# Kernel tuning notes

Measured on AMD Instinct MI355X. Metric: run time of the kernel, lower is better.

## Reference

```python
import jax, jax.numpy as jnp
import numpy as np

B, CIN, CGD, CE, G, H, W = 4, 256, 256, 64, 4, 80, 80
N = H * W
EPS = 1e-8


def _build_trees(guide_embed):
    # guide_embed: np [B, CE, N]. Minimum spanning tree on the 4-connected pixel
    # grid with edge cost exp(||e_u - e_v||^2) (exp is monotone -> same MST as
    # squared distance), then BFS order rooted at node 0.
    idx = np.arange(N).reshape(H, W)
    eu = np.concatenate([idx[:, :-1].ravel(), idx[:-1, :].ravel()])
    ev = np.concatenate([idx[:, 1:].ravel(), idx[1:, :].ravel()])
    orders, parents = [], []
    for b in range(B):
        fm = guide_embed[b]
        dist = ((fm[:, eu] - fm[:, ev]) ** 2).sum(0)
        root = np.arange(N)

        def find(x):
            while root[x] != x:
                root[x] = root[root[x]]
                x = root[x]
            return x

        adj = [[] for _ in range(N)]
        cnt = 0
        for e in np.argsort(dist, kind='stable'):
            a, b2 = find(eu[e]), find(ev[e])
            if a != b2:
                root[a] = b2
                adj[eu[e]].append(ev[e])
                adj[ev[e]].append(eu[e])
                cnt += 1
                if cnt == N - 1:
                    break
        order = np.zeros(N, np.int32)   # order[k] = node id at BFS position k
        ppos = np.zeros(N, np.int32)    # ppos[k]  = BFS position of parent of order[k]
        pos = np.zeros(N, np.int32)
        seen = np.zeros(N, bool)
        seen[0] = True
        head, tail = 0, 1
        while head < tail:
            x = order[head]
            for y in adj[x]:
                if not seen[y]:
                    seen[y] = True
                    order[tail] = y
                    pos[y] = tail
                    ppos[tail] = pos[x]
                    tail += 1
            head += 1
        orders.append(order)
        parents.append(ppos)
    return np.stack(orders), np.stack(parents)


def setup_inputs():
    key = jax.random.key(0)
    ks = jax.random.split(key, 7)
    feature = jax.random.normal(ks[0], (B, CIN, H, W), jnp.float32)
    guide = jax.random.normal(ks[1], (B, CGD, H, W), jnp.float32)
    # 1x1 convs == channel matmuls; std=0.01 per module init (conf/beta/gamma
    # are randomized instead of zero so the test is non-trivial)
    W_embed = 0.01 * jax.random.normal(ks[2], (CE, CIN), jnp.float32)
    W_conf = 0.05 * jax.random.normal(ks[3], (G, CIN), jnp.float32)
    W_guide = 0.01 * jax.random.normal(ks[4], (CE, CGD), jnp.float32)
    beta = 0.1 * jax.random.normal(ks[5], (G,), jnp.float32)
    gamma = 0.5 * jax.random.normal(ks[6], (1,), jnp.float32)
    # tree is built under no_grad in the original -> precompute (eval path: MST)
    ge = np.einsum('oc,bcn->bon', np.asarray(W_guide), np.asarray(guide).reshape(B, CGD, N))
    order, parent = _build_trees(ge)
    return {"feature": feature, "guide": guide, "W_embed": W_embed,
            "W_conf": W_conf, "W_guide": W_guide, "beta": beta, "gamma": gamma,
            "order": jnp.asarray(order), "parent": jnp.asarray(parent)}


def _group_edge_dist(x, order, parent):
    # x: [B, CE, N]; per-group squared L2 between each BFS node and its parent
    src = jnp.take_along_axis(x, order[:, None, :], axis=2)
    tgt = jnp.take_along_axis(src, parent[:, None, :], axis=2)
    d = (src - tgt) ** 2
    return d.reshape(B, G, CE // G, N).sum(axis=2)  # [B, G, N]


def _tree_filter(fs, w, parent):
    # fs: [N, G, C] node features in BFS order; w: [N, G] weight of edge to parent
    n = fs.shape[0]

    def up(agg, k):  # leaves -> root: subtree aggregation
        return agg.at[parent[k]].add(w[k][:, None] * agg[k]), None

    agg, _ = jax.lax.scan(up, fs, jnp.arange(n - 1, 0, -1))

    def down(out, k):  # root -> leaves: full-tree aggregation
        wk = w[k][:, None]
        return out.at[k].set(agg[k] + wk * (out[parent[k]] - wk * agg[k])), None

    out, _ = jax.lax.scan(down, agg, jnp.arange(1, n))
    return out


def reference(feature, guide, W_embed, W_conf, W_guide, beta, gamma, order, parent):
    f = feature.reshape(B, CIN, N)
    g = guide.reshape(B, CGD, N)  # adaptive_avg_pool2d to same HxW == identity
    embed = jnp.einsum('oc,bcn->bon', W_embed, f)
    guide_embed = jnp.einsum('oc,bcn->bon', W_guide, g)
    conf = jax.nn.sigmoid(jnp.einsum('gc,bcn->bgn', W_conf, f))  # [B, G, N]

    d_e = _group_edge_dist(embed, order, parent)
    d_g = _group_edge_dist(guide_embed, order, parent)
    # edge weight = exp(-d_embed) * exp(-d_guide) * exp(-beta^2) (self/att term)
    w = jnp.exp(-(d_e + d_g + (beta ** 2)[None, :, None]))  # [B, G, N] by BFS pos

    fg = f.reshape(B, G, CIN // G, N) * conf[:, :, None, :]  # conf-reweighted feat
    x = jnp.concatenate([fg, conf[:, :, None, :]], axis=2)   # filter feat & norm together
    xs = jnp.take_along_axis(x, order[:, None, None, :], axis=3)
    xs = xs.transpose(0, 3, 1, 2)                            # [B, N, G, Cpg+1]
    out = jax.vmap(_tree_filter)(xs, w.transpose(0, 2, 1), parent)
    inv = jnp.argsort(order, axis=1)                         # node -> BFS position
    out = jnp.take_along_axis(out, inv[:, :, None, None], axis=1)
    out = out.transpose(0, 2, 3, 1)                          # [B, G, Cpg+1, N]
    filt, norm = out[:, :, :-1, :], out[:, :, -1:, :]
    res = (filt / (EPS + norm)).reshape(B, CIN, N)
    return (gamma[0] * res + f).reshape(B, CIN, H, W)
```

## Files before the change

kernel.cpp:

```cpp
#include <hip/hip_runtime.h>
#include <math.h>

#define NB    4
#define CINC  256
#define NG    4
#define NPIX  6400
#define NROWS 132
#define CHG   65
#define TEPS  1e-8f
#define TP    128
#define KC    32
#define GT    256
#define SCH   5
#define SPITCH 6413
#define SWT   320
#define PT    640
#define LSC   512

typedef unsigned short u16;
typedef unsigned int   u32;

__global__ __launch_bounds__(PT) void prep_kernel(
    const int* __restrict__ order, const int* __restrict__ parent,
    u16* __restrict__ par16, int* __restrict__ ls,
    int* __restrict__ nl, int* __restrict__ inv)
{
  const int b = blockIdx.x;
  const int tid = threadIdx.x;
  const int* par = parent + b*NPIX;
  const int* ord = order + b*NPIX;
  __shared__ int lvl[NPIX];
  __shared__ int anc[NPIX];
  __shared__ int smax;

  #pragma unroll
  for (int it = 0; it < NPIX/PT; ++it) {
    int k = tid + it*PT;
    int p = par[k];
    lvl[k] = (k == 0) ? 0 : 1;
    anc[k] = p;
    inv[b*NPIX + ord[k]] = k;
    par16[b*NPIX + k] = (u16)p;
  }
  __syncthreads();

  for (int r = 0; r < 13; ++r) {
    int nlv[NPIX/PT], nan_[NPIX/PT];
    #pragma unroll
    for (int it = 0; it < NPIX/PT; ++it) {
      int k = tid + it*PT;
      int a = anc[k];
      nlv[it]  = lvl[k] + lvl[a];
      nan_[it] = anc[a];
    }
    __syncthreads();
    #pragma unroll
    for (int it = 0; it < NPIX/PT; ++it) {
      int k = tid + it*PT;
      lvl[k] = nlv[it];
      anc[k] = nan_[it];
    }
    __syncthreads();
  }

  if (tid == 0) smax = 0;
  __syncthreads();
  int m = 0;
  #pragma unroll
  for (int it = 0; it < NPIX/PT; ++it) m = max(m, lvl[tid + it*PT]);
  atomicMax(&smax, m);
  __syncthreads();
  if (tid == 0) {
    nl[b] = smax + 1;
    ls[b*(NPIX+2) + smax + 1] = NPIX;
  }
  #pragma unroll
  for (int it = 0; it < NPIX/PT; ++it) {
    int k = tid + it*PT;
    if (k == 0 || lvl[k] != lvl[k-1]) ls[b*(NPIX+2) + lvl[k]] = k;
  }
}

__global__ __launch_bounds__(GT) void gemm_kernel(
    const float* __restrict__ f, const float* __restrict__ g,
    const float* __restrict__ We, const float* __restrict__ Wc,
    const float* __restrict__ Wg, float* __restrict__ emb)
{
  const int b  = blockIdx.y;
  const int t0 = blockIdx.x * TP;
  const int tid = threadIdx.x;
  const int i = tid >> 4;
  const int j = tid & 15;

  __shared__ float fT[KC][TP];
  __shared__ float gT[KC][TP];
  __shared__ float wTt[KC][136];

  float acc[8][8];
  #pragma unroll
  for (int r = 0; r < 8; ++r)
    #pragma unroll
    for (int p = 0; p < 8; ++p) acc[r][p] = 0.f;
  float accc[8];
  #pragma unroll
  for (int p = 0; p < 8; ++p) accc[p] = 0.f;

  const float* fb = f + (size_t)b*CINC*NPIX;
  const float* gb = g + (size_t)b*CINC*NPIX;
  const float (*xT)[TP] = (i < 8) ? fT : gT;

  for (int kc = 0; kc < CINC; kc += KC) {
    {
      int kk = tid >> 3;
      int p  = (tid & 7) * 16;
      const float4* srcf = reinterpret_cast<const float4*>(fb + (size_t)(kc+kk)*NPIX + t0 + p);
      const float4* srcg = reinterpret_cast<const float4*>(gb + (size_t)(kc+kk)*NPIX + t0 + p);
      float4* df = reinterpret_cast<float4*>(&fT[kk][p]);
      float4* dg = reinterpret_cast<float4*>(&gT[kk][p]);
      #pragma unroll
      for (int q = 0; q < 4; ++q) { df[q] = srcf[q]; dg[q] = srcg[q]; }
    }
    for (int s = tid; s < 528; s += GT) {
      int r = s >> 2, kb0 = (s & 3) * 8;
      const float* wsrc;
      if (r < 64)       wsrc = We + r*CINC + kc + kb0;
      else if (r < 128) wsrc = Wg + (r-64)*CINC + kc + kb0;
      else              wsrc = Wc + (r-128)*CINC + kc + kb0;
      const float4* wv = reinterpret_cast<const float4*>(wsrc);
      float4 v0 = wv[0], v1 = wv[1];
      wTt[kb0+0][r]=v0.x; wTt[kb0+1][r]=v0.y; wTt[kb0+2][r]=v0.z; wTt[kb0+3][r]=v0.w;
      wTt[kb0+4][r]=v1.x; wTt[kb0+5][r]=v1.y; wTt[kb0+6][r]=v1.z; wTt[kb0+7][r]=v1.w;
    }
    __syncthreads();

    for (int kk = 0; kk < KC; ++kk) {
      float4 x0 = *reinterpret_cast<const float4*>(&xT[kk][4*j]);
      float4 x1 = *reinterpret_cast<const float4*>(&xT[kk][64 + 4*j]);
      float4 w0 = *reinterpret_cast<const float4*>(&wTt[kk][8*i]);
      float4 w1 = *reinterpret_cast<const float4*>(&wTt[kk][8*i + 4]);
#define FMA8(r, wv) \
      acc[r][0] += (wv)*x0.x; acc[r][1] += (wv)*x0.y; acc[r][2] += (wv)*x0.z; acc[r][3] += (wv)*x0.w; \
      acc[r][4] += (wv)*x1.x; acc[r][5] += (wv)*x1.y; acc[r][6] += (wv)*x1.z; acc[r][7] += (wv)*x1.w;
      FMA8(0, w0.x) FMA8(1, w0.y) FMA8(2, w0.z) FMA8(3, w0.w)
      FMA8(4, w1.x) FMA8(5, w1.y) FMA8(6, w1.z) FMA8(7, w1.w)
#undef FMA8
      if (i < 4) {
        float wcf = wTt[kk][128 + i];
        accc[0] += wcf*x0.x; accc[1] += wcf*x0.y; accc[2] += wcf*x0.z; accc[3] += wcf*x0.w;
        accc[4] += wcf*x1.x; accc[5] += wcf*x1.y; accc[6] += wcf*x1.z; accc[7] += wcf*x1.w;
      }
    }
    __syncthreads();
  }

  float* eb = emb + (size_t)b*NPIX*NROWS;
  #pragma unroll
  for (int p = 0; p < 8; ++p) {
    int n = t0 + ((p >> 2) * 64) + 4*j + (p & 3);
    float4 v0 = make_float4(acc[0][p], acc[1][p], acc[2][p], acc[3][p]);
    float4 v1 = make_float4(acc[4][p], acc[5][p], acc[6][p], acc[7][p]);
    float* base = eb + (size_t)n*NROWS + 8*i;
    *reinterpret_cast<float4*>(base)     = v0;
    *reinterpret_cast<float4*>(base + 4) = v1;
    if (i < 4) eb[(size_t)n*NROWS + 128 + i] = 1.f / (1.f + expf(-accc[p]));
  }
}

__global__ __launch_bounds__(256) void wdist_kernel(
    const float* __restrict__ emb, const int* __restrict__ order,
    const int* __restrict__ parent, const float* __restrict__ beta,
    u16* __restrict__ wq)
{
  int idx = blockIdx.x*256 + threadIdx.x;
  int b = idx / NPIX;
  int k = idx - b*NPIX;
  int n  = order[idx];
  int kp = parent[idx];
  int np = order[b*NPIX + kp];
  const float4* e0 = reinterpret_cast<const float4*>(emb + ((size_t)b*NPIX + n )*NROWS);
  const float4* e1 = reinterpret_cast<const float4*>(emb + ((size_t)b*NPIX + np)*NROWS);
  float d[NG] = {0.f, 0.f, 0.f, 0.f};
  #pragma unroll
  for (int q = 0; q < 32; ++q) {
    float4 a = e0[q], c = e1[q];
    int gg = (q & 15) >> 2;
    float t0 = a.x-c.x, t1 = a.y-c.y, t2 = a.z-c.z, t3 = a.w-c.w;
    d[gg] += t0*t0 + t1*t1 + t2*t2 + t3*t3;
  }
  #pragma unroll
  for (int gg = 0; gg < NG; ++gg) {
    float bg = beta[gg];
    float w = expf(-(d[gg] + bg*bg));
    wq[((size_t)(b*NG+gg))*NPIX + k] = (u16)(w*65535.f + 0.5f);
  }
}

__global__ __launch_bounds__(256) void gatherX_kernel(
    const float* __restrict__ f, const float* __restrict__ emb,
    const int* __restrict__ order, float* __restrict__ aggT)
{
  const int bid = blockIdx.x;
  const int pair = bid & 15, tile = bid >> 4;
  const int b = pair >> 2, g = pair & 3;
  const int k0 = tile * 128;
  const int tid = threadIdx.x;

  __shared__ int   s_ord[128];
  __shared__ float s_cf[128];
  if (tid < 128) {
    int n = order[b*NPIX + k0 + tid];
    s_ord[tid] = n;
    s_cf[tid]  = emb[((size_t)b*NPIX + n)*NROWS + 128 + g];
  }
  __syncthreads();

  const float* fb = f + (size_t)b*CINC*NPIX + (size_t)g*64*NPIX;
  float* dst = aggT + (size_t)(b*NG+g)*CHG*NPIX + k0;
  const int c0 = tid >> 7;
  const int j  = tid & 127;
  const int n  = s_ord[j];
  const float cf = s_cf[j];
  #pragma unroll 4
  for (int cc = c0; cc < 64; cc += 2) {
    dst[(size_t)cc*NPIX + j] = fb[(size_t)cc*NPIX + n] * cf;
  }
  if (tid < 128) dst[(size_t)64*NPIX + j] = cf;
}

__global__ __launch_bounds__(SWT, 1) void sweep_kernel(
    float* __restrict__ aggT, const u16* __restrict__ wq,
    const u16* __restrict__ par16, const int* __restrict__ ls,
    const int* __restrict__ nl)
{
  extern __shared__ char smem[];
  float* s_agg = (float*)smem;
  u32*  s_w32  = (u32*)(smem + 128264);
  u32*  s_p32  = (u32*)(smem + 128264 + 12800);
  int*  s_ls   = (int*)(smem + 128264 + 25600);
  u16*  s_w    = (u16*)s_w32;
  u16*  s_par  = (u16*)s_p32;

  const int bid = blockIdx.x;
  const int b = bid / (NG*13);
  const int r = bid - b*(NG*13);
  const int g = r / 13;
  const int ch0 = (r - g*13) * SCH;
  const int tid = threadIdx.x;
  const int ld = tid & 63;
  const int cw = tid >> 6;
  const int bg = b*NG + g;

  {
    const float4* src = reinterpret_cast<const float4*>(aggT + ((size_t)bg*CHG + ch0 + cw)*NPIX);
    float* dst = s_agg + cw*SPITCH;
    for (int i = ld; i < NPIX/4; i += 64) {
      float4 v = src[i];
      int k = i*4;
      dst[k] = v.x; dst[k+1] = v.y; dst[k+2] = v.z; dst[k+3] = v.w;
    }
  }
  {
    const u32* wsrc = reinterpret_cast<const u32*>(wq + (size_t)bg*NPIX);
    const u32* psrc = reinterpret_cast<const u32*>(par16 + (size_t)b*NPIX);
    for (int i = tid; i < NPIX/2; i += SWT) {
      s_w32[i] = wsrc[i];
      s_p32[i] = psrc[i];
    }
  }
  const int* lsb = ls + b*(NPIX+2);
  const int L = nl[b];
  for (int i = tid; i <= L && i < LSC; i += SWT) s_ls[i] = lsb[i];
  __syncthreads();

  const float qs = 1.0f/65535.0f;
  float* sa = s_agg + cw*SPITCH;
  auto LS = [&](int x) -> int { x = min(x, L); return (x < LSC) ? s_ls[x] : lsb[x]; };

  {
    int lev = L-2;
    int A = LS(lev), Bv = LS(lev+1), Cv = LS(lev+2);
    while (lev >= 0) {
      int nxt = (lev > 0) ? LS(lev-1) : 0;
      for (int k = Bv + ld; k < Cv; k += 64) {
        int p = s_par[k];
        float wv = (float)s_w[k] * qs;
        atomicAdd(&sa[p], wv * sa[k]);
      }
      asm volatile("" ::: "memory");
      Cv = Bv; Bv = A; A = nxt; --lev;
    }
  }

  {
    int lev = 1;
    int A = LS(1), Bv = LS(2);
    while (lev < L) {
      int nxt = LS(lev+2);
      for (int k = A + ld; k < Bv; k += 64) {
        int p = s_par[k];
        float wv = (float)s_w[k] * qs;
        float a  = sa[k];
        float op = sa[p];
        sa[k] = fmaf(wv, op - wv*a, a);
      }
      asm volatile("" ::: "memory");
      A = Bv; Bv = nxt; ++lev;
    }
  }

  __syncthreads();

  {
    float4* dst = reinterpret_cast<float4*>(aggT + ((size_t)bg*CHG + ch0 + cw)*NPIX);
    const float* srcp = s_agg + cw*SPITCH;
    for (int i = ld; i < NPIX/4; i += 64) {
      int k = i*4;
      dst[i] = make_float4(srcp[k], srcp[k+1], srcp[k+2], srcp[k+3]);
    }
  }
}

__global__ __launch_bounds__(256) void epilogue_kernel(
    const float* __restrict__ aggT, const int* __restrict__ inv,
    const float* __restrict__ f, const float* __restrict__ gamma,
    float* __restrict__ out)
{
  const int bid = blockIdx.x;
  const int b = bid & 3, tile = bid >> 2;
  const int n0 = tile * 64;
  const int tid = threadIdx.x;
  const int g = tid >> 6, j = tid & 63;

  __shared__ int s_k[64];
  if (tid < 64) s_k[tid] = inv[b*NPIX + n0 + tid];
  __syncthreads();

  const int k = s_k[j];
  const float* at = aggT + (size_t)(b*NG + g)*CHG*NPIX;
  const float rn = 1.f / (TEPS + at[(size_t)64*NPIX + k]);
  const float gam = gamma[0];
  const float* fb = f   + (size_t)b*CINC*NPIX + (size_t)g*64*NPIX;
  float*       ob = out + (size_t)b*CINC*NPIX + (size_t)g*64*NPIX;
  #pragma unroll 4
  for (int cc = 0; cc < 64; ++cc) {
    float val = at[(size_t)cc*NPIX + k];
    float fv  = fb[(size_t)cc*NPIX + n0 + j];
    ob[(size_t)cc*NPIX + n0 + j] = fmaf(gam, val*rn, fv);
  }
}

extern "C" void kernel_launch(void* const* d_in, const int* in_sizes, int n_in,
                              void* d_out, int out_size, void* d_ws, size_t ws_size,
                              hipStream_t stream)
{
  const float* f     = (const float*)d_in[0];
  const float* g     = (const float*)d_in[1];
  const float* We    = (const float*)d_in[2];
  const float* Wc    = (const float*)d_in[3];
  const float* Wg    = (const float*)d_in[4];
  const float* beta  = (const float*)d_in[5];
  const float* gamma = (const float*)d_in[6];
  const int* order   = (const int*)d_in[7];
  const int* parent  = (const int*)d_in[8];
  float* out = (float*)d_out;

  char* ws = (char*)d_ws;
  size_t off = 0;
  auto carve = [&](size_t bytes) -> void* {
    void* p = ws + off;
    off = (off + bytes + 255) & ~(size_t)255;
    return p;
  };
  float* emb = (float*)carve((size_t)NB*NPIX*NROWS*4);
  float* aggT= (float*)carve((size_t)NB*NG*CHG*NPIX*4);
  u16*  wq   = (u16*) carve((size_t)NB*NG*NPIX*2);
  u16*  par16= (u16*) carve((size_t)NB*NPIX*2);
  int*  ls   = (int*) carve((size_t)NB*(NPIX+2)*4);
  int*  nl   = (int*) carve((size_t)NB*4);
  int*  inv  = (int*) carve((size_t)NB*NPIX*4);

  const int sweep_lds = 128264 + 12800 + 12800 + 2048;
  hipFuncSetAttribute((const void*)sweep_kernel,
                      hipFuncAttributeMaxDynamicSharedMemorySize, sweep_lds);

  hipLaunchKernelGGL(prep_kernel,    dim3(NB),           dim3(PT), 0, stream,
                     order, parent, par16, ls, nl, inv);
  hipLaunchKernelGGL(gemm_kernel,    dim3(NPIX/TP, NB),  dim3(GT), 0, stream,
                     f, g, We, Wc, Wg, emb);
  hipLaunchKernelGGL(wdist_kernel,   dim3(NB*NPIX/256),  dim3(256), 0, stream,
                     emb, order, parent, beta, wq);
  hipLaunchKernelGGL(gatherX_kernel, dim3(16*(NPIX/128)),dim3(256), 0, stream,
                     f, emb, order, aggT);
  hipLaunchKernelGGL(sweep_kernel,   dim3(NB*NG*13),     dim3(SWT), sweep_lds, stream,
                     aggT, wq, par16, ls, nl);
  hipLaunchKernelGGL(epilogue_kernel,dim3((NPIX/64)*NB), dim3(256), 0, stream,
                     aggT, inv, f, gamma, out);
}
```

Measured before the change: 371.5 us.

## Process two tree levels per step using grandparent contributions and prefetch

The upward and downward tree-filter passes now handle two BFS levels per iteration instead of one. In the upward pass, nodes at the deeper level push weighted values to both their parent and their grandparent. In the downward pass, the deeper level is updated from the grandparent through a composed weight. This halves the number of serial level steps on deep MST trees. Parent indices and weights for the next iteration are also prefetched into registers. The cost is extra shared-memory atomics and loads per node, plus more register pressure.

```diff
diff --git a/kernel.cpp b/kernel.cpp
--- a/kernel.cpp
+++ b/kernel.cpp
@@ -277,34 +277,101 @@
   auto LS = [&](int x) -> int { x = min(x, L); return (x < LSC) ? s_ls[x] : lsb[x]; };
 
   {
-    int lev = L-2;
-    int A = LS(lev), Bv = LS(lev+1), Cv = LS(lev+2);
-    while (lev >= 0) {
-      int nxt = (lev > 0) ? LS(lev-1) : 0;
-      for (int k = Bv + ld; k < Cv; k += 64) {
-        int p = s_par[k];
-        float wv = (float)s_w[k] * qs;
-        atomicAdd(&sa[p], wv * sa[k]);
+    int t = L-2;
+    int sD = LS(t+1), eD = LS(t+2);
+    int sM = 0, eM = 0;
+    if (t >= 1) { sM = LS(t); eM = sD; }
+    int kD = sD + ld, kM = sM + ld;
+    bool aD = kD < eD, aM = kM < eM;
+    int pD=0, gpD=0, pM=0; float wD=0.f, wpD=0.f, wM=0.f;
+    if (aD) { pD = s_par[kD]; wD = (float)s_w[kD]*qs; gpD = s_par[pD]; wpD = (float)s_w[pD]*qs; }
+    if (aM) { pM = s_par[kM]; wM = (float)s_w[kM]*qs; }
+
+    while (t >= 0) {
+      int nt = t - 2;
+      int nsD=0, neD=0, nsM=0, neM=0;
+      if (nt >= 0) {
+        nsD = LS(nt+1); neD = LS(nt+2);
+        if (nt >= 1) { nsM = LS(nt); neM = nsD; }
+      }
+      float vD = aD ? sa[kD] : 0.f;
+      float vM = aM ? sa[kM] : 0.f;
+      int nkD = nsD + ld, nkM = nsM + ld;
+      bool naD = nkD < neD, naM = nkM < neM;
+      int npD=0, ngpD=0, npM=0; float nwD=0.f, nwpD=0.f, nwM=0.f;
+      if (naD) { npD = s_par[nkD]; nwD = (float)s_w[nkD]*qs; ngpD = s_par[npD]; nwpD = (float)s_w[npD]*qs; }
+      if (naM) { npM = s_par[nkM]; nwM = (float)s_w[nkM]*qs; }
+      for (int k = sM + 64 + ld; k < eM; k += 64) {
+        int p = s_par[k]; float w2 = (float)s_w[k]*qs;
+        atomicAdd(&sa[p], w2 * sa[k]);
+      }
+      if (aM) atomicAdd(&sa[pM], wM * vM);
+      if (aD) {
+        atomicAdd(&sa[pD], wD * vD);
+        if (t >= 1) atomicAdd(&sa[gpD], wD * wpD * vD);
+      }
+      for (int k = sD + 64 + ld; k < eD; k += 64) {
+        int p = s_par[k]; float w2 = (float)s_w[k]*qs;
+        float v = sa[k];
+        atomicAdd(&sa[p], w2 * v);
+        if (t >= 1) { float wp2 = (float)s_w[p]*qs; atomicAdd(&sa[s_par[p]], w2*wp2*v); }
       }
       asm volatile("" ::: "memory");
-      Cv = Bv; Bv = A; A = nxt; --lev;
+      sD=nsD; eD=neD; sM=nsM; eM=neM;
+      kD=nkD; kM=nkM; aD=naD; aM=naM;
+      pD=npD; gpD=ngpD; wD=nwD; wpD=nwpD; pM=npM; wM=nwM;
+      t = nt;
     }
   }
 
   {
-    int lev = 1;
-    int A = LS(1), Bv = LS(2);
-    while (lev < L) {
-      int nxt = LS(lev+2);
-      for (int k = A + ld; k < Bv; k += 64) {
-        int p = s_par[k];
-        float wv = (float)s_w[k] * qs;
-        float a  = sa[k];
-        float op = sa[p];
-        sa[k] = fmaf(wv, op - wv*a, a);
-      }
+    int t = 1;
+    int sS = LS(1), eS = LS(2);
+    int sD2 = 0, eD2 = 0;
+    if (2 <= L-1) { sD2 = eS; eD2 = LS(3); }
+    int kS = sS + ld, kD = sD2 + ld;
+    bool aS = kS < eS, aD = kD < eD2;
+    int pS=0, pD=0, gpD=0; float wS=0.f, wD=0.f, wpD=0.f;
+    if (aS) { pS = s_par[kS]; wS = (float)s_w[kS]*qs; }
+    if (aD) { pD = s_par[kD]; wD = (float)s_w[kD]*qs; gpD = s_par[pD]; wpD = (float)s_w[pD]*qs; }
+
+    while (t <= L-1) {
+      int nt = t + 2;
+      int nsS=0, neS=0, nsD=0, neD=0;
+      if (nt <= L-1) {
+        nsS = LS(nt); neS = LS(nt+1);
+        if (nt+1 <= L-1) { nsD = neS; neD = LS(nt+2); }
+      }
+      float aSv=0.f, oP=0.f, aDv=0.f, aPv=0.f, oGP=0.f;
+      if (aS) { aSv = sa[kS]; oP = sa[pS]; }
+      if (aD) { aDv = sa[kD]; aPv = sa[pD]; oGP = sa[gpD]; }
+      int nkS = nsS + ld, nkD = nsD + ld;
+      bool naS = nkS < neS, naD = nkD < neD;
+      int npS=0, npD=0, ngpD=0; float nwS=0.f, nwD=0.f, nwpD=0.f;
+      if (naS) { npS = s_par[nkS]; nwS = (float)s_w[nkS]*qs; }
+      if (naD) { npD = s_par[nkD]; nwD = (float)s_w[nkD]*qs; ngpD = s_par[npD]; nwpD = (float)s_w[npD]*qs; }
+      for (int k = sD2 + 64 + ld; k < eD2; k += 64) {
+        int p = s_par[k]; float wj = (float)s_w[k]*qs;
+        int gp = s_par[p]; float wp2 = (float)s_w[p]*qs;
+        float aj = sa[k], ap = sa[p], og = sa[gp];
+        float t1 = fmaf(wp2, og - wp2*ap, ap);
+        sa[k] = fmaf(wj, t1 - wj*aj, aj);
+      }
+      if (aD) {
+        float t1 = fmaf(wpD, oGP - wpD*aPv, aPv);
+        sa[kD] = fmaf(wD, t1 - wD*aDv, aDv);
+      }
+      for (int k = sS + 64 + ld; k < eS; k += 64) {
+        int p = s_par[k]; float wk = (float)s_w[k]*qs;
+        float ak = sa[k], op2 = sa[p];
+        sa[k] = fmaf(wk, op2 - wk*ak, ak);
+      }
+      if (aS) sa[kS] = fmaf(wS, oP - wS*aSv, aSv);
       asm volatile("" ::: "memory");
-      A = Bv; Bv = nxt; ++lev;
+      sS=nsS; eS=neS; sD2=nsD; eD2=neD;
+      kS=nkS; kD=nkD; aS=naS; aD=naD;
+      pS=npS; wS=nwS; pD=npD; gpD=ngpD; wD=nwD; wpD=nwpD;
+      t = nt;
     }
   }
 
```

Result: slower. 441.3 us (+18.8%).

## Fuse gather into tree sweep and early-exit pointer-jumping loop

Applied to the files above, without the earlier changes.

Removes the separate gatherX kernel. The sweep kernel now gathers conf-weighted features in BFS order straight from f and emb into shared memory, which drops one kernel launch and the write and re-read of the aggT staging buffer. The trade-off is that the gathers inside sweep are now scattered loads, repeated per block, with a strided conf read at stride NROWS, all running on only 208 blocks. The prep kernel's pointer-jumping loop also now exits early via __syncthreads_and once every ancestor reaches the root.

```diff
diff --git a/kernel.cpp b/kernel.cpp
--- a/kernel.cpp
+++ b/kernel.cpp
@@ -46,14 +46,16 @@
 
   for (int r = 0; r < 13; ++r) {
     int nlv[NPIX/PT], nan_[NPIX/PT];
+    int alldone = 1;
     #pragma unroll
     for (int it = 0; it < NPIX/PT; ++it) {
       int k = tid + it*PT;
       int a = anc[k];
+      alldone &= (a == 0);
       nlv[it]  = lvl[k] + lvl[a];
       nan_[it] = anc[a];
     }
-    __syncthreads();
+    if (__syncthreads_and(alldone)) break;
     #pragma unroll
     for (int it = 0; it < NPIX/PT; ++it) {
       int k = tid + it*PT;
@@ -195,42 +197,11 @@
   }
 }
 
-__global__ __launch_bounds__(256) void gatherX_kernel(
+__global__ __launch_bounds__(SWT, 1) void sweep_kernel(
     const float* __restrict__ f, const float* __restrict__ emb,
-    const int* __restrict__ order, float* __restrict__ aggT)
-{
-  const int bid = blockIdx.x;
-  const int pair = bid & 15, tile = bid >> 4;
-  const int b = pair >> 2, g = pair & 3;
-  const int k0 = tile * 128;
-  const int tid = threadIdx.x;
-
-  __shared__ int   s_ord[128];
-  __shared__ float s_cf[128];
-  if (tid < 128) {
-    int n = order[b*NPIX + k0 + tid];
-    s_ord[tid] = n;
-    s_cf[tid]  = emb[((size_t)b*NPIX + n)*NROWS + 128 + g];
-  }
-  __syncthreads();
-
-  const float* fb = f + (size_t)b*CINC*NPIX + (size_t)g*64*NPIX;
-  float* dst = aggT + (size_t)(b*NG+g)*CHG*NPIX + k0;
-  const int c0 = tid >> 7;
-  const int j  = tid & 127;
-  const int n  = s_ord[j];
-  const float cf = s_cf[j];
-  #pragma unroll 4
-  for (int cc = c0; cc < 64; cc += 2) {
-    dst[(size_t)cc*NPIX + j] = fb[(size_t)cc*NPIX + n] * cf;
-  }
-  if (tid < 128) dst[(size_t)64*NPIX + j] = cf;
-}
-
-__global__ __launch_bounds__(SWT, 1) void sweep_kernel(
-    float* __restrict__ aggT, const u16* __restrict__ wq,
-    const u16* __restrict__ par16, const int* __restrict__ ls,
-    const int* __restrict__ nl)
+    const int* __restrict__ order, float* __restrict__ aggT,
+    const u16* __restrict__ wq, const u16* __restrict__ par16,
+    const int* __restrict__ ls, const int* __restrict__ nl)
 {
   extern __shared__ char smem[];
   float* s_agg = (float*)smem;
@@ -251,12 +222,23 @@
   const int bg = b*NG + g;
 
   {
-    const float4* src = reinterpret_cast<const float4*>(aggT + ((size_t)bg*CHG + ch0 + cw)*NPIX);
+    const int c = ch0 + cw;
+    const int* ordb = order + b*NPIX;
+    const float* cfb = emb + (size_t)b*NPIX*NROWS + 128 + g;
     float* dst = s_agg + cw*SPITCH;
-    for (int i = ld; i < NPIX/4; i += 64) {
-      float4 v = src[i];
-      int k = i*4;
-      dst[k] = v.x; dst[k+1] = v.y; dst[k+2] = v.z; dst[k+3] = v.w;
+    if (c < 64) {
+      const float* fc = f + (size_t)b*CINC*NPIX + (size_t)(g*64 + c)*NPIX;
+      #pragma unroll 4
+      for (int k = ld; k < NPIX; k += 64) {
+        int n = ordb[k];
+        dst[k] = fc[n] * cfb[(size_t)n*NROWS];
+      }
+    } else {
+      #pragma unroll 4
+      for (int k = ld; k < NPIX; k += 64) {
+        int n = ordb[k];
+        dst[k] = cfb[(size_t)n*NROWS];
+      }
     }
   }
   {
@@ -389,10 +371,8 @@
                      f, g, We, Wc, Wg, emb);
   hipLaunchKernelGGL(wdist_kernel,   dim3(NB*NPIX/256),  dim3(256), 0, stream,
                      emb, order, parent, beta, wq);
-  hipLaunchKernelGGL(gatherX_kernel, dim3(16*(NPIX/128)),dim3(256), 0, stream,
-                     f, emb, order, aggT);
   hipLaunchKernelGGL(sweep_kernel,   dim3(NB*NG*13),     dim3(SWT), sweep_lds, stream,
-                     aggT, wq, par16, ls, nl);
+                     f, emb, order, aggT, wq, par16, ls, nl);
   hipLaunchKernelGGL(epilogue_kernel,dim3((NPIX/64)*NB), dim3(256), 0, stream,
                      aggT, inv, f, gamma, out);
 }
```

Measured after the change: 391.5 us. +5.4%, slower.

## Merge prep with GEMM and wdist with gather into shared launches

Applied to the files above, without the earlier changes.

Folds the tree-level prep work into extra blocks of the embedding GEMM kernel, and merges the edge-weight kernel with the feature gather kernel, cutting the launch count from six to four. Independent work now runs concurrently in one launch instead of serially. The prep path packs level and ancestor into one 32-bit LDS word and uses 256 threads instead of 640. Its pointer-jumping loop can now exit early once every ancestor reaches the root. In exchange, the prep blocks run with fewer threads and may become the tail of the combined kernel.

```diff
diff --git a/kernel.cpp b/kernel.cpp
--- a/kernel.cpp
+++ b/kernel.cpp
@@ -10,221 +10,218 @@
 #define TEPS  1e-8f
 #define TP    128
 #define KC    32
-#define GT    256
 #define SCH   5
 #define SPITCH 6413
 #define SWT   320
-#define PT    640
 #define LSC   512
 
 typedef unsigned short u16;
 typedef unsigned int   u32;
 
-__global__ __launch_bounds__(PT) void prep_kernel(
+__global__ __launch_bounds__(256) void gemm_prep_kernel(
+    const float* __restrict__ f, const float* __restrict__ g,
+    const float* __restrict__ We, const float* __restrict__ Wc,
+    const float* __restrict__ Wg, float* __restrict__ emb,
     const int* __restrict__ order, const int* __restrict__ parent,
     u16* __restrict__ par16, int* __restrict__ ls,
     int* __restrict__ nl, int* __restrict__ inv)
 {
-  const int b = blockIdx.x;
+  __shared__ __align__(16) char smem[50176];
+  __shared__ int smax;
+  const int bid = blockIdx.x;
   const int tid = threadIdx.x;
-  const int* par = parent + b*NPIX;
-  const int* ord = order + b*NPIX;
-  __shared__ int lvl[NPIX];
-  __shared__ int anc[NPIX];
-  __shared__ int smax;
-
-  #pragma unroll
-  for (int it = 0; it < NPIX/PT; ++it) {
-    int k = tid + it*PT;
-    int p = par[k];
-    lvl[k] = (k == 0) ? 0 : 1;
-    anc[k] = p;
-    inv[b*NPIX + ord[k]] = k;
-    par16[b*NPIX + k] = (u16)p;
-  }
-  __syncthreads();
-
-  for (int r = 0; r < 13; ++r) {
-    int nlv[NPIX/PT], nan_[NPIX/PT];
-    #pragma unroll
-    for (int it = 0; it < NPIX/PT; ++it) {
-      int k = tid + it*PT;
-      int a = anc[k];
-      nlv[it]  = lvl[k] + lvl[a];
-      nan_[it] = anc[a];
+
+  if (bid < 200) {
+    const int b  = bid / 50;
+    const int t0 = (bid - b*50) * TP;
+    const int i = tid >> 4;
+    const int j = tid & 15;
+
+    float (*fT)[TP]   = reinterpret_cast<float(*)[TP]>(smem);
+    float (*gT)[TP]   = reinterpret_cast<float(*)[TP]>(smem + 16384);
+    float (*wTt)[136] = reinterpret_cast<float(*)[136]>(smem + 32768);
+
+    float acc[8][8];
+    #pragma unroll
+    for (int r = 0; r < 8; ++r)
+      #pragma unroll
+      for (int p = 0; p < 8; ++p) acc[r][p] = 0.f;
+    float accc[8];
+    #pragma unroll
+    for (int p = 0; p < 8; ++p) accc[p] = 0.f;
+
+    const float* fb = f + (size_t)b*CINC*NPIX;
+    const float* gb = g + (size_t)b*CINC*NPIX;
+
+    for (int kc = 0; kc < CINC; kc += KC) {
+      {
+        int kk = tid >> 3;
+        int p  = (tid & 7) * 16;
+        const float4* srcf = reinterpret_cast<const float4*>(fb + (size_t)(kc+kk)*NPIX + t0 + p);
+        const float4* srcg = reinterpret_cast<const float4*>(gb + (size_t)(kc+kk)*NPIX + t0 + p);
+        float4* df = reinterpret_cast<float4*>(&fT[kk][p]);
+        float4* dg = reinterpret_cast<float4*>(&gT[kk][p]);
+        #pragma unroll
+        for (int q = 0; q < 4; ++q) { df[q] = srcf[q]; dg[q] = srcg[q]; }
+      }
+      for (int s = tid; s < 528; s += 256) {
+        int r = s >> 2, kb0 = (s & 3) * 8;
+        const float* wsrc;
+        if (r < 64)       wsrc = We + r*CINC + kc + kb0;
+        else if (r < 128) wsrc = Wg + (r-64)*CINC + kc + kb0;
+        else              wsrc = Wc + (r-128)*CINC + kc + kb0;
+        const float4* wv = reinterpret_cast<const float4*>(wsrc);
+        float4 v0 = wv[0], v1 = wv[1];
+        wTt[kb0+0][r]=v0.x; wTt[kb0+1][r]=v0.y; wTt[kb0+2][r]=v0.z; wTt[kb0+3][r]=v0.w;
+        wTt[kb0+4][r]=v1.x; wTt[kb0+5][r]=v1.y; wTt[kb0+6][r]=v1.z; wTt[kb0+7][r]=v1.w;
+      }
+      __syncthreads();
+
+      const float (*xT)[TP] = (i < 8) ? fT : gT;
+      for (int kk = 0; kk < KC; ++kk) {
+        float4 x0 = *reinterpret_cast<const float4*>(&xT[kk][4*j]);
+        float4 x1 = *reinterpret_cast<const float4*>(&xT[kk][64 + 4*j]);
+        float4 w0 = *reinterpret_cast<const float4*>(&wTt[kk][8*i]);
+        float4 w1 = *reinterpret_cast<const float4*>(&wTt[kk][8*i + 4]);
+#define FMA8(r, wv) \
+        acc[r][0] += (wv)*x0.x; acc[r][1] += (wv)*x0.y; acc[r][2] += (wv)*x0.z; acc[r][3] += (wv)*x0.w; \
+        acc[r][4] += (wv)*x1.x; acc[r][5] += (wv)*x1.y; acc[r][6] += (wv)*x1.z; acc[r][7] += (wv)*x1.w;
+        FMA8(0, w0.x) FMA8(1, w0.y) FMA8(2, w0.z) FMA8(3, w0.w)
+        FMA8(4, w1.x) FMA8(5, w1.y) FMA8(6, w1.z) FMA8(7, w1.w)
+#undef FMA8
+        if (i < 4) {
+          float wcf = wTt[kk][128 + i];
+          accc[0] += wcf*x0.x; accc[1] += wcf*x0.y; accc[2] += wcf*x0.z; accc[3] += wcf*x0.w;
+          accc[4] += wcf*x1.x; accc[5] += wcf*x1.y; accc[6] += wcf*x1.z; accc[7] += wcf*x1.w;
+        }
+      }
+      __syncthreads();
+    }
+
+    float* eb = emb + (size_t)b*NPIX*NROWS;
+    #pragma unroll
+    for (int p = 0; p < 8; ++p) {
+      int n = t0 + ((p >> 2) * 64) + 4*j + (p & 3);
+      float4 v0 = make_float4(acc[0][p], acc[1][p], acc[2][p], acc[3][p]);
+      float4 v1 = make_float4(acc[4][p], acc[5][p], acc[6][p], acc[7][p]);
+      float* base = eb + (size_t)n*NROWS + 8*i;
+      *reinterpret_cast<float4*>(base)     = v0;
+      *reinterpret_cast<float4*>(base + 4) = v1;
+      if (i < 4) eb[(size_t)n*NROWS + 128 + i] = 1.f / (1.f + expf(-accc[p]));
+    }
+  } else {
+    const int b = bid - 200;
+    const int* par = parent + b*NPIX;
+    const int* ord = order + b*NPIX;
+    u32* pk = reinterpret_cast<u32*>(smem);
+
+    #pragma unroll
+    for (int it = 0; it < NPIX/256; ++it) {
+      int k = tid + it*256;
+      int p = par[k];
+      pk[k] = ((u32)p << 16) | (k == 0 ? 0u : 1u);
+      inv[b*NPIX + ord[k]] = k;
+      par16[b*NPIX + k] = (u16)p;
     }
     __syncthreads();
-    #pragma unroll
-    for (int it = 0; it < NPIX/PT; ++it) {
-      int k = tid + it*PT;
-      lvl[k] = nlv[it];
-      anc[k] = nan_[it];
-    }
+
+    for (int r = 0; r < 13; ++r) {
+      u32 nv[NPIX/256];
+      int done = 1;
+      #pragma unroll
+      for (int it = 0; it < NPIX/256; ++it) {
+        int k = tid + it*256;
+        u32 w = pk[k];
+        u32 a = w >> 16;
+        done &= (a == 0u);
+        u32 pw = pk[a];
+        nv[it] = (pw & 0xffff0000u) | ((w + pw) & 0xffffu);
+      }
+      if (__syncthreads_and(done)) break;
+      #pragma unroll
+      for (int it = 0; it < NPIX/256; ++it) pk[tid + it*256] = nv[it];
+      __syncthreads();
+    }
+
+    if (tid == 0) smax = 0;
     __syncthreads();
-  }
-
-  if (tid == 0) smax = 0;
-  __syncthreads();
-  int m = 0;
-  #pragma unroll
-  for (int it = 0; it < NPIX/PT; ++it) m = max(m, lvl[tid + it*PT]);
-  atomicMax(&smax, m);
-  __syncthreads();
-  if (tid == 0) {
-    nl[b] = smax + 1;
-    ls[b*(NPIX+2) + smax + 1] = NPIX;
-  }
-  #pragma unroll
-  for (int it = 0; it < NPIX/PT; ++it) {
-    int k = tid + it*PT;
-    if (k == 0 || lvl[k] != lvl[k-1]) ls[b*(NPIX+2) + lvl[k]] = k;
-  }
-}
-
-__global__ __launch_bounds__(GT) void gemm_kernel(
-    const float* __restrict__ f, const float* __restrict__ g,
-    const float* __restrict__ We, const float* __restrict__ Wc,
-    const float* __restrict__ Wg, float* __restrict__ emb)
-{
-  const int b  = blockIdx.y;
-  const int t0 = blockIdx.x * TP;
-  const int tid = threadIdx.x;
-  const int i = tid >> 4;
-  const int j = tid & 15;
-
-  __shared__ float fT[KC][TP];
-  __shared__ float gT[KC][TP];
-  __shared__ float wTt[KC][136];
-
-  float acc[8][8];
-  #pragma unroll
-  for (int r = 0; r < 8; ++r)
-    #pragma unroll
-    for (int p = 0; p < 8; ++p) acc[r][p] = 0.f;
-  float accc[8];
-  #pragma unroll
-  for (int p = 0; p < 8; ++p) accc[p] = 0.f;
-
-  const float* fb = f + (size_t)b*CINC*NPIX;
-  const float* gb = g + (size_t)b*CINC*NPIX;
-  const float (*xT)[TP] = (i < 8) ? fT : gT;
-
-  for (int kc = 0; kc < CINC; kc += KC) {
-    {
-      int kk = tid >> 3;
-      int p  = (tid & 7) * 16;
-      const float4* srcf = reinterpret_cast<const float4*>(fb + (size_t)(kc+kk)*NPIX + t0 + p);
-      const float4* srcg = reinterpret_cast<const float4*>(gb + (size_t)(kc+kk)*NPIX + t0 + p);
-      float4* df = reinterpret_cast<float4*>(&fT[kk][p]);
-      float4* dg = reinterpret_cast<float4*>(&gT[kk][p]);
-      #pragma unroll
-      for (int q = 0; q < 4; ++q) { df[q] = srcf[q]; dg[q] = srcg[q]; }
-    }
-    for (int s = tid; s < 528; s += GT) {
-      int r = s >> 2, kb0 = (s & 3) * 8;
-      const float* wsrc;
-      if (r < 64)       wsrc = We + r*CINC + kc + kb0;
-      else if (r < 128) wsrc = Wg + (r-64)*CINC + kc + kb0;
-      else              wsrc = Wc + (r-128)*CINC + kc + kb0;
-      const float4* wv = reinterpret_cast<const float4*>(wsrc);
-      float4 v0 = wv[0], v1 = wv[1];
-      wTt[kb0+0][r]=v0.x; wTt[kb0+1][r]=v0.y; wTt[kb0+2][r]=v0.z; wTt[kb0+3][r]=v0.w;
-      wTt[kb0+4][r]=v1.x; wTt[kb0+5][r]=v1.y; wTt[kb0+6][r]=v1.z; wTt[kb0+7][r]=v1.w;
-    }
+    int m = 0;
+    #pragma unroll
+    for (int it = 0; it < NPIX/256; ++it) m = max(m, (int)(pk[tid + it*256] & 0xffffu));
+    atomicMax(&smax, m);
     __syncthreads();
-
-    for (int kk = 0; kk < KC; ++kk) {
-      float4 x0 = *reinterpret_cast<const float4*>(&xT[kk][4*j]);
-      float4 x1 = *reinterpret_cast<const float4*>(&xT[kk][64 + 4*j]);
-      float4 w0 = *reinterpret_cast<const float4*>(&wTt[kk][8*i]);
-      float4 w1 = *reinterpret_cast<const float4*>(&wTt[kk][8*i + 4]);
-#define FMA8(r, wv) \
-      acc[r][0] += (wv)*x0.x; acc[r][1] += (wv)*x0.y; acc[r][2] += (wv)*x0.z; acc[r][3] += (wv)*x0.w; \
-      acc[r][4] += (wv)*x1.x; acc[r][5] += (wv)*x1.y; acc[r][6] += (wv)*x1.z; acc[r][7] += (wv)*x1.w;
-      FMA8(0, w0.x) FMA8(1, w0.y) FMA8(2, w0.z) FMA8(3, w0.w)
-      FMA8(4, w1.x) FMA8(5, w1.y) FMA8(6, w1.z) FMA8(7, w1.w)
-#undef FMA8
-      if (i < 4) {
-        float wcf = wTt[kk][128 + i];
-        accc[0] += wcf*x0.x; accc[1] += wcf*x0.y; accc[2] += wcf*x0.z; accc[3] += wcf*x0.w;
-        accc[4] += wcf*x1.x; accc[5] += wcf*x1.y; accc[6] += wcf*x1.z; accc[7] += wcf*x1.w;
-      }
-    }
-    __syncthreads();
-  }
-
-  float* eb = emb + (size_t)b*NPIX*NROWS;
-  #pragma unroll
-  for (int p = 0; p < 8; ++p) {
-    int n = t0 + ((p >> 2) * 64) + 4*j + (p & 3);
-    float4 v0 = make_float4(acc[0][p], acc[1][p], acc[2][p], acc[3][p]);
-    float4 v1 = make_float4(acc[4][p], acc[5][p], acc[6][p], acc[7][p]);
-    float* base = eb + (size_t)n*NROWS + 8*i;
-    *reinterpret_cast<float4*>(base)     = v0;
-    *reinterpret_cast<float4*>(base + 4) = v1;
-    if (i < 4) eb[(size_t)n*NROWS + 128 + i] = 1.f / (1.f + expf(-accc[p]));
-  }
-}
-
-__global__ __launch_bounds__(256) void wdist_kernel(
+    if (tid == 0) {
+      nl[b] = smax + 1;
+      ls[b*(NPIX+2) + smax + 1] = NPIX;
+    }
+    #pragma unroll
+    for (int it = 0; it < NPIX/256; ++it) {
+      int k = tid + it*256;
+      int lv = (int)(pk[k] & 0xffffu);
+      if (k == 0 || lv != (int)(pk[k-1] & 0xffffu)) ls[b*(NPIX+2) + lv] = k;
+    }
+  }
+}
+
+__global__ __launch_bounds__(256) void wgx_kernel(
     const float* __restrict__ emb, const int* __restrict__ order,
     const int* __restrict__ parent, const float* __restrict__ beta,
-    u16* __restrict__ wq)
-{
-  int idx = blockIdx.x*256 + threadIdx.x;
-  int b = idx / NPIX;
-  int k = idx - b*NPIX;
-  int n  = order[idx];
-  int kp = parent[idx];
-  int np = order[b*NPIX + kp];
-  const float4* e0 = reinterpret_cast<const float4*>(emb + ((size_t)b*NPIX + n )*NROWS);
-  const float4* e1 = reinterpret_cast<const float4*>(emb + ((size_t)b*NPIX + np)*NROWS);
-  float d[NG] = {0.f, 0.f, 0.f, 0.f};
-  #pragma unroll
-  for (int q = 0; q < 32; ++q) {
-    float4 a = e0[q], c = e1[q];
-    int gg = (q & 15) >> 2;
-    float t0 = a.x-c.x, t1 = a.y-c.y, t2 = a.z-c.z, t3 = a.w-c.w;
-    d[gg] += t0*t0 + t1*t1 + t2*t2 + t3*t3;
-  }
-  #pragma unroll
-  for (int gg = 0; gg < NG; ++gg) {
-    float bg = beta[gg];
-    float w = expf(-(d[gg] + bg*bg));
-    wq[((size_t)(b*NG+gg))*NPIX + k] = (u16)(w*65535.f + 0.5f);
-  }
-}
-
-__global__ __launch_bounds__(256) void gatherX_kernel(
-    const float* __restrict__ f, const float* __restrict__ emb,
-    const int* __restrict__ order, float* __restrict__ aggT)
+    const float* __restrict__ f, u16* __restrict__ wq,
+    float* __restrict__ aggT)
 {
   const int bid = blockIdx.x;
-  const int pair = bid & 15, tile = bid >> 4;
-  const int b = pair >> 2, g = pair & 3;
-  const int k0 = tile * 128;
   const int tid = threadIdx.x;
-
   __shared__ int   s_ord[128];
   __shared__ float s_cf[128];
-  if (tid < 128) {
-    int n = order[b*NPIX + k0 + tid];
-    s_ord[tid] = n;
-    s_cf[tid]  = emb[((size_t)b*NPIX + n)*NROWS + 128 + g];
-  }
-  __syncthreads();
-
-  const float* fb = f + (size_t)b*CINC*NPIX + (size_t)g*64*NPIX;
-  float* dst = aggT + (size_t)(b*NG+g)*CHG*NPIX + k0;
-  const int c0 = tid >> 7;
-  const int j  = tid & 127;
-  const int n  = s_ord[j];
-  const float cf = s_cf[j];
-  #pragma unroll 4
-  for (int cc = c0; cc < 64; cc += 2) {
-    dst[(size_t)cc*NPIX + j] = fb[(size_t)cc*NPIX + n] * cf;
-  }
-  if (tid < 128) dst[(size_t)64*NPIX + j] = cf;
+
+  if (bid < 100) {
+    int idx = bid*256 + tid;
+    int b = idx / NPIX;
+    int k = idx - b*NPIX;
+    int n  = order[idx];
+    int kp = parent[idx];
+    int np = order[b*NPIX + kp];
+    const float4* e0 = reinterpret_cast<const float4*>(emb + ((size_t)b*NPIX + n )*NROWS);
+    const float4* e1 = reinterpret_cast<const float4*>(emb + ((size_t)b*NPIX + np)*NROWS);
+    float d[NG] = {0.f, 0.f, 0.f, 0.f};
+    #pragma unroll
+    for (int q = 0; q < 32; ++q) {
+      float4 a = e0[q], c = e1[q];
+      int gg = (q & 15) >> 2;
+      float t0 = a.x-c.x, t1 = a.y-c.y, t2 = a.z-c.z, t3 = a.w-c.w;
+      d[gg] += t0*t0 + t1*t1 + t2*t2 + t3*t3;
+    }
+    #pragma unroll
+    for (int gg = 0; gg < NG; ++gg) {
+      float bg = beta[gg];
+      float w = expf(-(d[gg] + bg*bg));
+      wq[((size_t)(b*NG+gg))*NPIX + k] = (u16)(w*65535.f + 0.5f);
+    }
+  } else {
+    const int r = bid - 100;
+    const int pair = r & 15, tile = r >> 4;
+    const int b = pair >> 2, g = pair & 3;
+    const int k0 = tile * 128;
+
+    if (tid < 128) {
+      int n = order[b*NPIX + k0 + tid];
+      s_ord[tid] = n;
+      s_cf[tid]  = emb[((size_t)b*NPIX + n)*NROWS + 128 + g];
+    }
+    __syncthreads();
+
+    const float* fb = f + (size_t)b*CINC*NPIX + (size_t)g*64*NPIX;
+    float* dst = aggT + (size_t)(b*NG+g)*CHG*NPIX + k0;
+    const int c0 = tid >> 7;
+    const int j  = tid & 127;
+    const int n  = s_ord[j];
+    const float cf = s_cf[j];
+    #pragma unroll 4
+    for (int cc = c0; cc < 64; cc += 2) {
+      dst[(size_t)cc*NPIX + j] = fb[(size_t)cc*NPIX + n] * cf;
+    }
+    if (tid < 128) dst[(size_t)64*NPIX + j] = cf;
+  }
 }
 
 __global__ __launch_bounds__(SWT, 1) void sweep_kernel(
@@ -383,16 +380,12 @@
   hipFuncSetAttribute((const void*)sweep_kernel,
                       hipFuncAttributeMaxDynamicSharedMemorySize, sweep_lds);
 
-  hipLaunchKernelGGL(prep_kernel,    dim3(NB),           dim3(PT), 0, stream,
-                     order, parent, par16, ls, nl, inv);
-  hipLaunchKernelGGL(gemm_kernel,    dim3(NPIX/TP, NB),  dim3(GT), 0, stream,
-                     f, g, We, Wc, Wg, emb);
-  hipLaunchKernelGGL(wdist_kernel,   dim3(NB*NPIX/256),  dim3(256), 0, stream,
-                     emb, order, parent, beta, wq);
-  hipLaunchKernelGGL(gatherX_kernel, dim3(16*(NPIX/128)),dim3(256), 0, stream,
-                     f, emb, order, aggT);
-  hipLaunchKernelGGL(sweep_kernel,   dim3(NB*NG*13),     dim3(SWT), sweep_lds, stream,
+  hipLaunchKernelGGL(gemm_prep_kernel, dim3(204),          dim3(256), 0, stream,
+                     f, g, We, Wc, Wg, emb, order, parent, par16, ls, nl, inv);
+  hipLaunchKernelGGL(wgx_kernel,       dim3(900),          dim3(256), 0, stream,
+                     emb, order, parent, beta, f, wq, aggT);
+  hipLaunchKernelGGL(sweep_kernel,     dim3(NB*NG*13),     dim3(SWT), sweep_lds, stream,
                      aggT, wq, par16, ls, nl);
-  hipLaunchKernelGGL(epilogue_kernel,dim3((NPIX/64)*NB), dim3(256), 0, stream,
+  hipLaunchKernelGGL(epilogue_kernel,  dim3((NPIX/64)*NB), dim3(256), 0, stream,
                      aggT, inv, f, gamma, out);
 }
```

Result: faster. 350.0 us (-5.8%).
